# Kernel tuning notes

Measured on AMD Instinct MI355X. Metric: run time of the kernel, lower is better.

The kernel has to match this reference:

```python
import jax, jax.numpy as jnp
import numpy as np

K_EDE = 10.0   # self.k
T_EDE = 0.1    # self.t
BN_EPS = 1e-5
T_A = 576.0    # 3*3*64, hardcoded in my_bn1/my_bn2


def qfn(x, prec):
    # dorefa-style round quantizer with straight-through gradient
    n = float(2 ** prec - 1)
    return x + jax.lax.stop_gradient(jnp.round(x * n) / n - x)


@jax.custom_vjp
def binary_quantize(x):
    return jnp.sign(x)


def _bq_fwd(x):
    return jnp.sign(x), x


def _bq_bwd(x, g):
    # IR-Net EDE backward: k * t * (1 - tanh(x*t)^2)
    return (K_EDE * T_EDE * (1.0 - jnp.tanh(x * T_EDE) ** 2) * g,)


binary_quantize.defvjp(_bq_fwd, _bq_bwd)


def _clip_T(x):
    T = jnp.maximum(jnp.abs(x.min()), jnp.abs(x.max()))
    return jax.lax.stop_gradient(jnp.clip(T, 1e-10, 255.0))


def quantize_conv_act(x, prec):
    # my_quantize_conv: clamp to [-T, T], scale to [-1,1], qfn (no rescale by T)
    T = _clip_T(x)
    return qfn(jnp.clip(x, -T, T) / T, prec)


def quantize(x, prec):
    # my_quantize: same but rescaled back by T
    T = _clip_T(x)
    return qfn(jnp.clip(x, -T, T) / T, prec) * T


def ir_conv2d(a, w, stride):
    # IR-Net 1w8a IRConv2d: per-out-channel normalize, binarize (sign), power-of-2 scale
    co = w.shape[0]
    wf = w.reshape(co, -1)
    bw = (w - wf.mean(1)[:, None, None, None]) / jnp.std(wf, axis=1, ddof=1)[:, None, None, None]
    sw = jax.lax.stop_gradient(
        2.0 ** jnp.round(jnp.log2(jnp.abs(bw.reshape(co, -1)).mean(1)))
    )[:, None, None, None]
    bw = binary_quantize(bw) * sw
    return jax.lax.conv_general_dilated(
        a, bw, window_strides=(stride, stride), padding=[(1, 1), (1, 1)],
        dimension_numbers=('NCHW', 'OIHW', 'NCHW'))


def bn_as_quantized_affine(x, gamma, beta, mean, var):
    # my_bn1/my_bn2 (eval mode): BN folded into per-channel scale+bias.
    # The original builds a CxC diagonal 1x1 conv; since off-diagonal entries are 0,
    # both the quantization stats (max|.|) and the conv reduce exactly to this
    # per-channel affine, which is the faithful fused form.
    std = jnp.sqrt(var + BN_EPS)
    w = gamma / std
    b = beta - w * mean
    qw = quantize(w, 3)
    qb = quantize(b, 12)
    aq = qfn(x / T_A, 10) * T_A  # my_quantize_activation(input, 10, T_a)
    return aq * qw[None, :, None, None] + qb[None, :, None, None]


def _block(x, w1, w2, g1, b1, m1, v1, g2, b2, m2, v2):
    xq = quantize_conv_act(x, 3)
    out = ir_conv2d(xq, w1, 1)
    out = bn_as_quantized_affine(out, g1, b1, m1, v1) + xq  # identity shortcut
    out = jnp.clip(out, -1.0, 1.0)  # hardtanh
    x1 = quantize_conv_act(out, 3)
    out = ir_conv2d(x1, w2, 1)
    out = bn_as_quantized_affine(out, g2, b2, m2, v2) + x1
    return jnp.clip(out, -1.0, 1.0)


def setup_inputs() -> dict:
    key = jax.random.key(0)
    ks = jax.random.split(key, 11)
    B, C, H, W = 128, 64, 56, 56
    return {
        'x': jax.random.normal(ks[0], (B, C, H, W), jnp.float32),
        'w1': jax.random.normal(ks[1], (C, C, 3, 3), jnp.float32) * 0.1,
        'w2': jax.random.normal(ks[2], (C, C, 3, 3), jnp.float32) * 0.1,
        'g1': jax.random.uniform(ks[3], (C,), jnp.float32, 0.5, 1.5),
        'b1': jax.random.normal(ks[4], (C,), jnp.float32) * 0.1,
        'm1': jax.random.normal(ks[5], (C,), jnp.float32) * 0.1,
        'v1': jax.random.uniform(ks[6], (C,), jnp.float32, 0.5, 1.5),
        'g2': jax.random.uniform(ks[7], (C,), jnp.float32, 0.5, 1.5),
        'b2': jax.random.normal(ks[8], (C,), jnp.float32) * 0.1,
        'm2': jax.random.normal(ks[9], (C,), jnp.float32) * 0.1,
        'v2': jax.random.uniform(ks[10], (C,), jnp.float32, 0.5, 1.5),
    }


def reference(x, w1, w2, g1, b1, m1, v1, g2, b2, m2, v2):
    return _block(x, w1, w2, g1, b1, m1, v1, g2, b2, m2, v2)
```

## Files before the change

kernel.cpp:

```cpp
#include <hip/hip_runtime.h>
#include <stdint.h>

typedef int v4i   __attribute__((ext_vector_type(4)));
typedef int v16i  __attribute__((ext_vector_type(16)));

#define B_    128
#define C_    64
#define H_    56
#define W_    56
#define HW_   3136
#define NELEM (B_*C_*HW_)

#define OFF_K0   0
#define OFF_K1   ((size_t)NELEM)
#define OFF_WB   ((size_t)2*NELEM)
#define OFF_PAR  (OFF_WB + 2*4*9*64*16)
#define OFF_MAX  (OFF_PAR + 384*4)

__device__ __forceinline__ float pw_reduce64(float r) {
    r = __fadd_rn(r, __shfl_xor(r, 1, 64));
    r = __fadd_rn(r, __shfl_xor(r, 2, 64));
    r = __fadd_rn(r, __shfl_xor(r, 4, 64));
    r = __fadd_rn(r, __shfl_xor(r, 8, 64));
    r = __fadd_rn(r, __shfl_xor(r, 16, 64));
    r = __fadd_rn(r, __shfl_xor(r, 32, 64));
    return r;
}

__global__ void k_pre(const float* __restrict__ x, unsigned* __restrict__ maxbits,
                      const float* __restrict__ w1, const float* __restrict__ w2,
                      int8_t* __restrict__ wb, float* __restrict__ par,
                      const float* __restrict__ g1, const float* __restrict__ bb1,
                      const float* __restrict__ mm1, const float* __restrict__ vv1,
                      const float* __restrict__ g2, const float* __restrict__ bb2,
                      const float* __restrict__ mm2, const float* __restrict__ vv2) {
    __shared__ float smax[4];
    const int b = blockIdx.x;
    const int tid = threadIdx.x;
    if (b < 1024) {
        float m = 0.f;
        const int n4 = NELEM / 4;
        for (int i = b * 256 + tid; i < n4; i += 1024 * 256) {
            float4 v = ((const float4*)x)[i];
            m = fmaxf(m, fmaxf(fmaxf(fabsf(v.x), fabsf(v.y)), fmaxf(fabsf(v.z), fabsf(v.w))));
        }
        for (int off = 32; off; off >>= 1) m = fmaxf(m, __shfl_down(m, off, 64));
        if ((tid & 63) == 0) smax[tid >> 6] = m;
        __syncthreads();
        if (tid == 0) {
            float mm = fmaxf(fmaxf(smax[0], smax[1]), fmaxf(smax[2], smax[3]));
            atomicMax(maxbits, __float_as_uint(mm));
        }
    } else if (b < 1056) {
        const int idx = (b - 1024) * 4 + (tid >> 6);
        const int layer = idx >> 6, co = idx & 63;
        const int lane = tid & 63;
        const float* w = (layer ? w2 : w1) + (size_t)co * 576;
        const int base = (lane >> 3) * 72 + (lane & 7);

        float v[9];
#pragma unroll
        for (int i = 0; i < 9; i++) v[i] = w[base + 8 * i];

        float s = v[0];
#pragma unroll
        for (int i = 1; i < 9; i++) s = __fadd_rn(s, v[i]);
        const float mean = __fdiv_rn(pw_reduce64(s), 576.0f);

        float d0 = __fsub_rn(v[0], mean);
        float sq = __fmul_rn(d0, d0);
#pragma unroll
        for (int i = 1; i < 9; i++) {
            float d = __fsub_rn(v[i], mean);
            sq = __fadd_rn(sq, __fmul_rn(d, d));
        }
        const float sig = __fsqrt_rn(__fdiv_rn(pw_reduce64(sq), 575.0f));

        float sa = fabsf(__fdiv_rn(__fsub_rn(v[0], mean), sig));
#pragma unroll
        for (int i = 1; i < 9; i++)
            sa = __fadd_rn(sa, fabsf(__fdiv_rn(__fsub_rn(v[i], mean), sig)));
        const float ma = __fdiv_rn(pw_reduce64(sa), 576.0f);
        const float p  = rintf(log2f(ma));
        if (lane == 0) par[256 + layer * 64 + co] = __fdiv_rn(exp2f(p), 7.0f);

#pragma unroll
        for (int i = 0; i < 9; i++) {
            int ig = base + 8 * i;
            float d = __fsub_rn(v[i], mean);
            int8_t sg = (d > 0.0f) ? (int8_t)1 : ((d < 0.0f) ? (int8_t)-1 : (int8_t)0);
            int ci = ig / 9, tp = ig % 9;
            wb[((((size_t)layer * 4 + (ci >> 4)) * 9 + tp) * 64 + co) * 16 + (ci & 15)] = sg;
        }
    } else {
        if (tid < 128) {
            const int layer = tid >> 6;
            const int c = tid & 63;
            const float* g  = layer ? g2  : g1;
            const float* be = layer ? bb2 : bb1;
            const float* mu = layer ? mm2 : mm1;
            const float* va = layer ? vv2 : vv1;
            const float stdv = __fsqrt_rn(__fadd_rn(va[c], 1e-5f));
            const float w = __fdiv_rn(g[c], stdv);
            const float bb = __fsub_rn(be[c], __fmul_rn(w, mu[c]));
            float aw = fabsf(w), ab = fabsf(bb);
            for (int off = 32; off; off >>= 1) {
                aw = fmaxf(aw, __shfl_xor(aw, off, 64));
                ab = fmaxf(ab, __shfl_xor(ab, off, 64));
            }
            const float Tw = fminf(fmaxf(aw, 1e-10f), 255.0f);
            const float Tb = fminf(fmaxf(ab, 1e-10f), 255.0f);
            {
                float vq = __fdiv_rn(fminf(fmaxf(w, -Tw), Tw), Tw);
                float r  = rintf(__fmul_rn(vq, 7.0f));
                float qf = __fadd_rn(vq, __fsub_rn(__fdiv_rn(r, 7.0f), vq));
                par[layer * 64 + c] = __fmul_rn(qf, Tw);
            }
            {
                float vq = __fdiv_rn(fminf(fmaxf(bb, -Tb), Tb), Tb);
                float r  = rintf(__fmul_rn(vq, 4095.0f));
                float qf = __fadd_rn(vq, __fsub_rn(__fdiv_rn(r, 4095.0f), vq));
                par[128 + layer * 64 + c] = __fmul_rn(qf, Tb);
            }
        }
    }
}

__global__ void k_quant(const float* __restrict__ x, const unsigned* __restrict__ maxbits,
                        int8_t* __restrict__ k8) {
    __shared__ unsigned tile[56 * 17];
    const int n = blockIdx.x / H_;
    const int y = blockIdx.x % H_;
    const float T = fminf(fmaxf(__uint_as_float(*maxbits), 1e-10f), 255.0f);
    const double dinv = 1.0 / (double)T;
    const int t = threadIdx.x;
    if (t < 224) {
        const int cb = t / 14, xb = t % 14;
        const float* src = x + ((size_t)(n * 64 + 4 * cb)) * HW_ + y * 56 + 4 * xb;
        int kq[4][4];
#pragma unroll
        for (int i = 0; i < 4; i++) {
            float4 v = *(const float4*)(src + (size_t)i * HW_);
            const float e[4] = {v.x, v.y, v.z, v.w};
#pragma unroll
            for (int j = 0; j < 4; j++) {
                const float tc = fminf(fmaxf(e[j], -T), T);
                const float u  = (float)((double)tc * dinv);
                kq[i][j] = (int)rintf(__fmul_rn(u, 7.0f));
            }
        }
#pragma unroll
        for (int j = 0; j < 4; j++) {
            const unsigned d = (kq[0][j] & 255) | ((kq[1][j] & 255) << 8) |
                               ((kq[2][j] & 255) << 16) | ((unsigned)(kq[3][j] & 255) << 24);
            tile[(4 * xb + j) * 17 + cb] = d;
        }
    }
    __syncthreads();
    unsigned* dst = (unsigned*)(k8 + ((size_t)(n * 56 + y)) * 56 * 64);
    for (int u = t; u < 896; u += 256)
        dst[u] = tile[(u >> 4) * 17 + (u & 15)];
}

#define EPI_CHAIN(S_, scf_, xqv_, qwf_, qbf_, OUT_)                         \
    {   const float Sf_ = (float)(S_);                                      \
        const float convf_ = __fmul_rn(Sf_, scf_);                          \
        const float xb_ = (float)((double)convf_ * (1.0 / 576.0));          \
        const float rr_ = rintf(__fmul_rn(xb_, 1023.0f));                   \
        const float q1_ = (float)((double)rr_ * (1.0 / 1023.0));            \
        const float aq_ = __fmul_rn(q1_, 576.0f);                           \
        float vv_ = __fadd_rn(__fadd_rn(__fmul_rn(aq_, qwf_), qbf_), xqv_); \
        OUT_ = fminf(fmaxf(vv_, -1.0f), 1.0f); }

__global__ __launch_bounds__(448, 2) void k_fused(const int8_t* __restrict__ k0,
                                                  const int8_t* __restrict__ wb,
                                                  const float* __restrict__ par,
                                                  float* __restrict__ fout) {
    __shared__ __align__(16) int8_t wsm[2 * 4 * 9 * 64 * 16];
    __shared__ __align__(16) int8_t k0b[4 * 8 * 58 * 16];
    __shared__ __align__(16) int8_t x1b[4 * 8 * 58 * 16];
    __shared__ float lut7[16];
    const int n = blockIdx.x >> 1;
    const int b = (blockIdx.x & 1) * 28;
    const int tid = threadIdx.x;
    const int wv = tid >> 6, lane = tid & 63;
    const int mbase = wv * 32;
    const int ml = lane & 31;
    const int khalf = lane >> 5;
    const int m = mbase + ml;
    const int ym = m / 56, cm = m % 56;

    for (int u = tid; u < 4608; u += 448)
        *(int4*)(wsm + u * 16) = *(const int4*)(wb + (size_t)u * 16);
    for (int u = tid; u < 1392; u += 448) {
        const int q = u & 3, vv = u >> 2;
        const int rr = vv / 58, xp = vv % 58;
        const int r = b - 2 + rr, xg = xp - 1;
        int4 val = {0, 0, 0, 0};
        if (r >= 0 && r < 56 && xg >= 0 && xg < 56)
            val = *(const int4*)(k0 + (((size_t)(n * 56 + r)) * 56 + xg) * 64 + q * 16);
        *(int4*)(k0b + (((q * 8 + ((r + 2) & 7)) * 58 + xp) << 4)) = val;
    }
    if (tid < 64) {
        const int q = tid & 3, slot = (tid >> 2) & 7, xs = (tid >> 5) & 1;
        *(int4*)(x1b + (((q * 8 + slot) * 58 + xs * 57) << 4)) = (int4){0, 0, 0, 0};
    }
    if (tid < 15) lut7[tid] = __fdiv_rn((float)(tid - 7), 7.0f);
    __syncthreads();

    float qwf1[2], qbf1[2], scf1[2], qwf2[2], qbf2[2], scf2[2];
#pragma unroll
    for (int t = 0; t < 2; t++) {
        const int co = ml + t * 32;
        qwf1[t] = par[co];        qbf1[t] = par[128 + co]; scf1[t] = par[256 + co];
        qwf2[t] = par[64 + co];   qbf2[t] = par[192 + co]; scf2[t] = par[320 + co];
    }

    int4 pre[3];
#pragma unroll 1
    for (int i = 0; i < 8; ++i) {
        if (i < 7) {
            const int R0 = b + 4 * i + 4;
#pragma unroll
            for (int it = 0; it < 3; ++it) {
                const int u = tid + it * 448;
                int4 val = {0, 0, 0, 0};
                if (u < 928) {
                    const int q = u & 3, vv = u >> 2;
                    const int rr = vv / 58, xp = vv % 58;
                    const int r = R0 + rr, xg = xp - 1;
                    if (r >= 0 && r < 56 && xg >= 0 && xg < 56)
                        val = *(const int4*)(k0 + (((size_t)(n * 56 + r)) * 56 + xg) * 64 + q * 16);
                }
                pre[it] = val;
            }
        }
        const int y1base = b - 1 + 4 * i;
        {
            v16i acc0, acc1;
#pragma unroll
            for (int z = 0; z < 16; z++) { acc0[z] = 0; acc1[z] = 0; }
            __builtin_amdgcn_s_setprio(1);
#pragma unroll
            for (int s = 0; s < 9; s++) {
                const int ky = s / 3, kx = s % 3;
                const int arow = y1base + ym + ky - 1;
                const int aslot = (arow + 2) & 7;
#pragma unroll
                for (int kb = 0; kb < 2; kb++) {
                    const int q = khalf + 2 * kb;
                    v4i a  = *(const v4i*)(k0b + (((q * 8 + aslot) * 58 + cm + kx) << 4));
                    v4i b0 = *(const v4i*)(wsm + (((q * 9 + s) * 64 + ml) << 4));
                    v4i b1 = *(const v4i*)(wsm + (((q * 9 + s) * 64 + 32 + ml) << 4));
                    acc0 = __builtin_amdgcn_mfma_i32_32x32x32_i8(a, b0, acc0, 0, 0, 0);
                    acc1 = __builtin_amdgcn_mfma_i32_32x32x32_i8(a, b1, acc1, 0, 0, 0);
                }
            }
            __builtin_amdgcn_s_setprio(0);
#pragma unroll
            for (int t = 0; t < 2; t++) {
                const int co = ml + t * 32;
                const float qwf = qwf1[t], qbf = qbf1[t], scf = scf1[t];
                const int qc = co >> 4, cl = co & 15;
                const int clw = cl & ~3, cb8 = (cl & 3) * 8;
#pragma unroll
                for (int g = 0; g < 4; g++) {
                    const int mb = mbase + 8 * g + 4 * khalf;
                    const int rl = mb / 56, c0 = mb % 56;
                    const int y1g = y1base + rl;
                    const bool vrow = (y1g >= 0) && (y1g <= 55);
                    const bool wen  = (y1g <= b + 28);
                    const int ksl = (y1g + 2) & 7;
                    const int xsl = (y1g + 1) & 7;
                    const int resb = (qc * 8 + ksl) * 58 + c0 + 1;
                    const int outb = (qc * 8 + xsl) * 58 + c0 + 1;
#pragma unroll
                    for (int i4 = 0; i4 < 4; i4++) {
                        const int S = t ? acc1[4 * g + i4] : acc0[4 * g + i4];
                        const unsigned wd = *(const unsigned*)(k0b + ((resb + i4) << 4) + clw);
                        const int kc = (int)(int8_t)(wd >> cb8);
                        const float xqv = lut7[kc + 7];
                        float val; EPI_CHAIN(S, scf, xqv, qwf, qbf, val);
                        int k2 = (int)rintf(__fmul_rn(val, 7.0f));
                        if (!vrow) k2 = 0;
                        const unsigned lowb = (unsigned)(k2 & 255);
                        const unsigned hib  = (unsigned)__shfl_xor((int)(lowb << 8), 1, 64);
                        if (wen && (ml & 1) == 0)
                            *(uint16_t*)(x1b + ((outb + i4) << 4) + (cl & ~1)) =
                                (uint16_t)(lowb | hib);
                    }
                }
            }
        }
        __syncthreads();

        if (i < 7) {
            const int R0 = b + 4 * i + 4;
#pragma unroll
            for (int it = 0; it < 3; ++it) {
                const int u = tid + it * 448;
                if (u < 928) {
                    const int q = u & 3, vv = u >> 2;
                    const int rr = vv / 58, xp = vv % 58;
                    const int r = R0 + rr;
                    *(int4*)(k0b + (((q * 8 + ((r + 2) & 7)) * 58 + xp) << 4)) = pre[it];
                }
            }
        }
        if (i >= 1) {
            const int y2base = b + 4 * (i - 1);
            v16i acc0, acc1;
#pragma unroll
            for (int z = 0; z < 16; z++) { acc0[z] = 0; acc1[z] = 0; }
            __builtin_amdgcn_s_setprio(1);
#pragma unroll
            for (int s = 0; s < 9; s++) {
                const int ky = s / 3, kx = s % 3;
                const int arow = y2base + ym + ky - 1;
                const int aslot = (arow + 1) & 7;
#pragma unroll
                for (int kb = 0; kb < 2; kb++) {
                    const int q = khalf + 2 * kb;
                    v4i a  = *(const v4i*)(x1b + (((q * 8 + aslot) * 58 + cm + kx) << 4));
                    v4i b0 = *(const v4i*)(wsm + 36864 + (((q * 9 + s) * 64 + ml) << 4));
                    v4i b1 = *(const v4i*)(wsm + 36864 + (((q * 9 + s) * 64 + 32 + ml) << 4));
                    acc0 = __builtin_amdgcn_mfma_i32_32x32x32_i8(a, b0, acc0, 0, 0, 0);
                    acc1 = __builtin_amdgcn_mfma_i32_32x32x32_i8(a, b1, acc1, 0, 0, 0);
                }
            }
            __builtin_amdgcn_s_setprio(0);
#pragma unroll
            for (int t = 0; t < 2; t++) {
                const int co = ml + t * 32;
                const float qwf = qwf2[t], qbf = qbf2[t], scf = scf2[t];
                const int qc = co >> 4, cl = co & 15;
                const int clw = cl & ~3, cb8 = (cl & 3) * 8;
#pragma unroll
                for (int g = 0; g < 4; g++) {
                    const int mb = mbase + 8 * g + 4 * khalf;
                    const int rl = mb / 56, c0 = mb % 56;
                    const int y2g = y2base + rl;
                    const int xsl = (y2g + 1) & 7;
                    const int resb = (qc * 8 + xsl) * 58 + c0 + 1;
                    float vals[4];
#pragma unroll
                    for (int i4 = 0; i4 < 4; i4++) {
                        const int S = t ? acc1[4 * g + i4] : acc0[4 * g + i4];
                        const unsigned wd = *(const unsigned*)(x1b + ((resb + i4) << 4) + clw);
                        const int kc = (int)(int8_t)(wd >> cb8);
                        const float xqv = lut7[kc + 7];
                        EPI_CHAIN(S, scf, xqv, qwf, qbf, vals[i4]);
                    }
                    float4 o = make_float4(vals[0], vals[1], vals[2], vals[3]);
                    *(float4*)(fout + ((size_t)(n * 64 + co)) * HW_ + y2g * 56 + c0) = o;
                }
            }
        }
        if (i < 7) __syncthreads();
    }
}

extern "C" void kernel_launch(void* const* d_in, const int* in_sizes, int n_in,
                              void* d_out, int out_size, void* d_ws, size_t ws_size,
                              hipStream_t stream) {
    const float* x  = (const float*)d_in[0];
    const float* w1 = (const float*)d_in[1];
    const float* w2 = (const float*)d_in[2];
    const float* g1 = (const float*)d_in[3];
    const float* b1 = (const float*)d_in[4];
    const float* m1 = (const float*)d_in[5];
    const float* v1 = (const float*)d_in[6];
    const float* g2 = (const float*)d_in[7];
    const float* b2 = (const float*)d_in[8];
    const float* m2 = (const float*)d_in[9];
    const float* v2 = (const float*)d_in[10];

    char* ws = (char*)d_ws;
    int8_t*  k0  = (int8_t*)(ws + OFF_K0);
    int8_t*  wbp = (int8_t*)(ws + OFF_WB);
    float*   par = (float*)(ws + OFF_PAR);
    unsigned* mx = (unsigned*)(ws + OFF_MAX);

    hipMemsetAsync(mx, 0, 4, stream);
    k_pre<<<1057, 256, 0, stream>>>(x, mx, w1, w2, wbp, par,
                                    g1, b1, m1, v1, g2, b2, m2, v2);
    k_quant<<<B_ * H_, 256, 0, stream>>>(x, mx, k0);
    k_fused<<<B_ * 2, 448, 0, stream>>>(k0, wbp, par, (float*)d_out);
}
```

Before: 306.4 us.

## Fuse activation quantization into main conv kernel, dropping int8 intermediate

Removes the separate quantization kernel and its int8 global buffer; the fused conv kernel now loads float input rows directly, quantizes them to 3-bit codes in registers, and writes packed bytes into the shared-memory ring buffer, including prefetch of upcoming rows. This removes the launch and the int8 write/read round trip through global memory. In exchange each block reads 4x wider float data including halo rows, and the in-loop prefetch now carries quantization arithmetic and more registers.

```diff
diff --git a/kernel.cpp b/kernel.cpp
--- a/kernel.cpp
+++ b/kernel.cpp
@@ -11,8 +11,6 @@
 #define HW_   3136
 #define NELEM (B_*C_*HW_)
 
-#define OFF_K0   0
-#define OFF_K1   ((size_t)NELEM)
 #define OFF_WB   ((size_t)2*NELEM)
 #define OFF_PAR  (OFF_WB + 2*4*9*64*16)
 #define OFF_MAX  (OFF_PAR + 384*4)
@@ -126,17 +124,11 @@
     }
 }
 
-__global__ void k_quant(const float* __restrict__ x, const unsigned* __restrict__ maxbits,
-                        int8_t* __restrict__ k8) {
-    __shared__ unsigned tile[56 * 17];
-    const int n = blockIdx.x / H_;
-    const int y = blockIdx.x % H_;
-    const float T = fminf(fmaxf(__uint_as_float(*maxbits), 1e-10f), 255.0f);
-    const double dinv = 1.0 / (double)T;
-    const int t = threadIdx.x;
-    if (t < 224) {
-        const int cb = t / 14, xb = t % 14;
-        const float* src = x + ((size_t)(n * 64 + 4 * cb)) * HW_ + y * 56 + 4 * xb;
+__device__ __forceinline__ void quant_task(const float* __restrict__ x, int n, int r,
+                                           int cb4, int xj, float T, double dinv,
+                                           unsigned d[4]) {
+    if (r >= 0 && r < 56) {
+        const float* src = x + ((size_t)(n * 64 + 4 * cb4)) * HW_ + r * 56 + 4 * xj;
         int kq[4][4];
 #pragma unroll
         for (int i = 0; i < 4; i++) {
@@ -150,16 +142,21 @@
             }
         }
 #pragma unroll
-        for (int j = 0; j < 4; j++) {
-            const unsigned d = (kq[0][j] & 255) | ((kq[1][j] & 255) << 8) |
-                               ((kq[2][j] & 255) << 16) | ((unsigned)(kq[3][j] & 255) << 24);
-            tile[(4 * xb + j) * 17 + cb] = d;
-        }
-    }
-    __syncthreads();
-    unsigned* dst = (unsigned*)(k8 + ((size_t)(n * 56 + y)) * 56 * 64);
-    for (int u = t; u < 896; u += 256)
-        dst[u] = tile[(u >> 4) * 17 + (u & 15)];
+        for (int j = 0; j < 4; j++)
+            d[j] = (kq[0][j] & 255) | ((kq[1][j] & 255) << 8) |
+                   ((kq[2][j] & 255) << 16) | ((unsigned)(kq[3][j] & 255) << 24);
+    } else {
+#pragma unroll
+        for (int j = 0; j < 4; j++) d[j] = 0;
+    }
+}
+
+__device__ __forceinline__ void quant_write(int8_t* k0b, int r, int cb4, int xj,
+                                            const unsigned d[4]) {
+    int8_t* base = k0b + ((((cb4 >> 2) * 8 + ((r + 2) & 7)) * 58) << 4) + (cb4 & 3) * 4;
+#pragma unroll
+    for (int j = 0; j < 4; j++)
+        *(unsigned*)(base + ((4 * xj + 1 + j) << 4)) = d[j];
 }
 
 #define EPI_CHAIN(S_, scf_, xqv_, qwf_, qbf_, OUT_)                         \
@@ -172,7 +169,8 @@
         float vv_ = __fadd_rn(__fadd_rn(__fmul_rn(aq_, qwf_), qbf_), xqv_); \
         OUT_ = fminf(fmaxf(vv_, -1.0f), 1.0f); }
 
-__global__ __launch_bounds__(448, 2) void k_fused(const int8_t* __restrict__ k0,
+__global__ __launch_bounds__(448, 2) void k_fused(const float* __restrict__ x,
+                                                  const unsigned* __restrict__ maxbits,
                                                   const int8_t* __restrict__ wb,
                                                   const float* __restrict__ par,
                                                   float* __restrict__ fout) {
@@ -190,22 +188,29 @@
     const int m = mbase + ml;
     const int ym = m / 56, cm = m % 56;
 
+    const float T = fminf(fmaxf(__uint_as_float(*maxbits), 1e-10f), 255.0f);
+    const double dinv = 1.0 / (double)T;
+
     for (int u = tid; u < 4608; u += 448)
         *(int4*)(wsm + u * 16) = *(const int4*)(wb + (size_t)u * 16);
-    for (int u = tid; u < 1392; u += 448) {
-        const int q = u & 3, vv = u >> 2;
-        const int rr = vv / 58, xp = vv % 58;
-        const int r = b - 2 + rr, xg = xp - 1;
-        int4 val = {0, 0, 0, 0};
-        if (r >= 0 && r < 56 && xg >= 0 && xg < 56)
-            val = *(const int4*)(k0 + (((size_t)(n * 56 + r)) * 56 + xg) * 64 + q * 16);
-        *(int4*)(k0b + (((q * 8 + ((r + 2) & 7)) * 58 + xp) << 4)) = val;
-    }
     if (tid < 64) {
         const int q = tid & 3, slot = (tid >> 2) & 7, xs = (tid >> 5) & 1;
         *(int4*)(x1b + (((q * 8 + slot) * 58 + xs * 57) << 4)) = (int4){0, 0, 0, 0};
     }
+    if (tid >= 64 && tid < 128) {
+        const int t2 = tid - 64;
+        const int q = t2 & 3, slot = (t2 >> 2) & 7, xs = (t2 >> 5) & 1;
+        *(int4*)(k0b + (((q * 8 + slot) * 58 + xs * 57) << 4)) = (int4){0, 0, 0, 0};
+    }
     if (tid < 15) lut7[tid] = __fdiv_rn((float)(tid - 7), 7.0f);
+    for (int tt = tid; tt < 1344; tt += 448) {
+        const int r6 = tt / 224, rem = tt % 224;
+        const int cb4 = rem / 14, xj = rem % 14;
+        const int r = b - 2 + r6;
+        unsigned d[4];
+        quant_task(x, n, r, cb4, xj, T, dinv, d);
+        quant_write(k0b, r, cb4, xj, d);
+    }
     __syncthreads();
 
     float qwf1[2], qbf1[2], scf1[2], qwf2[2], qbf2[2], scf2[2];
@@ -216,23 +221,17 @@
         qwf2[t] = par[64 + co];   qbf2[t] = par[192 + co]; scf2[t] = par[320 + co];
     }
 
-    int4 pre[3];
+    unsigned pd[2][4];
 #pragma unroll 1
     for (int i = 0; i < 8; ++i) {
         if (i < 7) {
             const int R0 = b + 4 * i + 4;
 #pragma unroll
-            for (int it = 0; it < 3; ++it) {
-                const int u = tid + it * 448;
-                int4 val = {0, 0, 0, 0};
-                if (u < 928) {
-                    const int q = u & 3, vv = u >> 2;
-                    const int rr = vv / 58, xp = vv % 58;
-                    const int r = R0 + rr, xg = xp - 1;
-                    if (r >= 0 && r < 56 && xg >= 0 && xg < 56)
-                        val = *(const int4*)(k0 + (((size_t)(n * 56 + r)) * 56 + xg) * 64 + q * 16);
-                }
-                pre[it] = val;
+            for (int e2 = 0; e2 < 2; ++e2) {
+                const int tt = tid + e2 * 448;
+                const int r4 = tt / 224, rem = tt % 224;
+                const int cb4 = rem / 14, xj = rem % 14;
+                quant_task(x, n, R0 + r4, cb4, xj, T, dinv, pd[e2]);
             }
         }
         const int y1base = b - 1 + 4 * i;
@@ -297,14 +296,11 @@
         if (i < 7) {
             const int R0 = b + 4 * i + 4;
 #pragma unroll
-            for (int it = 0; it < 3; ++it) {
-                const int u = tid + it * 448;
-                if (u < 928) {
-                    const int q = u & 3, vv = u >> 2;
-                    const int rr = vv / 58, xp = vv % 58;
-                    const int r = R0 + rr;
-                    *(int4*)(k0b + (((q * 8 + ((r + 2) & 7)) * 58 + xp) << 4)) = pre[it];
-                }
+            for (int e2 = 0; e2 < 2; ++e2) {
+                const int tt = tid + e2 * 448;
+                const int r4 = tt / 224, rem = tt % 224;
+                const int cb4 = rem / 14, xj = rem % 14;
+                quant_write(k0b, R0 + r4, cb4, xj, pd[e2]);
             }
         }
         if (i >= 1) {
@@ -376,7 +372,6 @@
     const float* v2 = (const float*)d_in[10];
 
     char* ws = (char*)d_ws;
-    int8_t*  k0  = (int8_t*)(ws + OFF_K0);
     int8_t*  wbp = (int8_t*)(ws + OFF_WB);
     float*   par = (float*)(ws + OFF_PAR);
     unsigned* mx = (unsigned*)(ws + OFF_MAX);
@@ -384,6 +379,5 @@
     hipMemsetAsync(mx, 0, 4, stream);
     k_pre<<<1057, 256, 0, stream>>>(x, mx, w1, w2, wbp, par,
                                     g1, b1, m1, v1, g2, b2, m2, v2);
-    k_quant<<<B_ * H_, 256, 0, stream>>>(x, mx, k0);
-    k_fused<<<B_ * 2, 448, 0, stream>>>(k0, wbp, par, (float*)d_out);
-}
+    k_fused<<<B_ * 2, 448, 0, stream>>>(x, mx, wbp, par, (float*)d_out);
+}
```

New measurement: 286.6 us. 6.4% less time.
